# Kernel tuning notes

Hardware: AMD Instinct MI355X
Metric: run time of the kernel (lower is better)

## Reference

```python
import jax, jax.numpy as jnp
import numpy as np

DIM_MODEL = 2048
H, DK, DV, L = 16, 128, 128, 2048
LN_EPS = 1e-5


def setup_inputs() -> dict:
    key = jax.random.key(0)
    ks = jax.random.split(key, 8)
    # xavier-ish scale for weights so softmax logits stay sane
    w_scale = (2.0 / (DIM_MODEL + DK)) ** 0.5
    q = jax.random.normal(ks[0], (1, L, DIM_MODEL), dtype=jnp.float32)
    k = jax.random.normal(ks[1], (1, L, DIM_MODEL), dtype=jnp.float32)
    v = jax.random.normal(ks[2], (1, L, DIM_MODEL), dtype=jnp.float32)
    Wq = jax.random.normal(ks[3], (H, DIM_MODEL, DK), dtype=jnp.float32) * w_scale
    Wk = jax.random.normal(ks[4], (H, DIM_MODEL, DK), dtype=jnp.float32) * w_scale
    Wv = jax.random.normal(ks[5], (H, DIM_MODEL, DV), dtype=jnp.float32) * w_scale
    proj_w = jax.random.normal(ks[6], (H * DV, DIM_MODEL), dtype=jnp.float32) * (1.0 / (H * DV) ** 0.5)
    proj_b = jnp.zeros((DIM_MODEL,), dtype=jnp.float32)
    ln_g = jnp.ones((DIM_MODEL,), dtype=jnp.float32)
    ln_b = jnp.zeros((DIM_MODEL,), dtype=jnp.float32)
    return {"q": q, "k": k, "v": v, "Wq": Wq, "Wk": Wk, "Wv": Wv,
            "proj_w": proj_w, "proj_b": proj_b, "ln_g": ln_g, "ln_b": ln_b}


def reference(q, k, v, Wq, Wk, Wv, proj_w, proj_b, ln_g, ln_b):
    # batch must be 1 (enforced by torch.bmm shape rules in the source)
    residual = q  # (1, L, D)
    qs, kv, vv = q[0], k[0], v[0]  # (L, D)
    dim_model = qs.shape[-1]
    temper = jnp.asarray(dim_model, qs.dtype) ** 0.5  # sqrt(dim_model), NOT sqrt(dk)
    qh = jnp.einsum('ld,hdk->hlk', qs, Wq)  # (H, L, dk)
    kh = jnp.einsum('ld,hdk->hlk', kv, Wk)  # (H, L, dk)
    vh = jnp.einsum('ld,hdv->hlv', vv, Wv)  # (H, L, dv)
    scores = jnp.einsum('hqk,hmk->hqm', qh, kh) / temper  # (H, Lq, Lk)
    # faithful quirk: softmax over dim=1 (the QUERY axis)
    attn = jax.nn.softmax(scores, axis=1)
    # attn_dropout / dropout are identity in eval mode
    out = jnp.einsum('hqm,hmv->hqv', attn, vh)  # (H, Lq, dv)
    # cat(split(out, batch=1, dim=0), dim=-1) == move head axis into features
    Lq = out.shape[1]
    out = jnp.transpose(out, (1, 0, 2)).reshape(Lq, -1)  # (Lq, H*dv)
    out = out @ proj_w + proj_b  # (Lq, dim_model)
    y = out[None] + residual  # (1, Lq, D)
    mu = jnp.mean(y, axis=-1, keepdims=True)
    var = jnp.mean((y - mu) ** 2, axis=-1, keepdims=True)
    y = (y - mu) * jax.lax.rsqrt(var + LN_EPS) * ln_g + ln_b
    return (y, attn)
```

## Files before the change

### kernel.cpp

```cpp
#include <hip/hip_runtime.h>
#include <stdint.h>

#define L 2048
#define DMODEL 2048
#define NH 16

typedef __bf16 bf16x8 __attribute__((ext_vector_type(8)));
typedef float f32x4 __attribute__((ext_vector_type(4)));
typedef short s16x4 __attribute__((ext_vector_type(4)));

__device__ __forceinline__ unsigned short f2bf(float f) {
    union { float f; unsigned int i; } w; w.f = f;
    unsigned int u = w.i;
    unsigned int r = u + 0x7fffu + ((u >> 16) & 1u);
    return (unsigned short)(r >> 16);
}

__device__ __forceinline__ void gload_lds16(const unsigned short* g, unsigned short* l) {
    __builtin_amdgcn_global_load_lds(
        (const __attribute__((address_space(1))) void*)g,
        (__attribute__((address_space(3))) void*)l, 16, 0, 0);
}

template<int CMODE, int AMODE, int BM, int BK, int PSM>
__global__ __launch_bounds__(256, 2)
void gemm_bt(const void* Av,
             const unsigned short* __restrict__ B,
             void* __restrict__ C,
             int M, int N, int K, int lda, int ldb, int ldc,
             long long sA, long long sB, long long sC, float alpha,
             const float* __restrict__ Mg, const float* __restrict__ iLg,
             float* Awr, float* __restrict__ pPart)
{
    static_assert(AMODE != 2 || BM == 64, "softmax-A path assumes BM==64");
    static_assert(PSM == 0 || BM == 128, "PSM partials assume BM==128");
    constexpr int KC8 = BK / 8;
    constexpr int CA  = BM * BK / 2048;
    constexpr int CB  = BK / 16;
    constexpr int MFR = BM / 32;
    constexpr int KG  = BK / 32;

    __shared__ unsigned short As[2][BM * BK];
    __shared__ unsigned short Bs[2][128 * BK];

    const int tid  = threadIdx.x;
    const int wave = tid >> 6;
    const int lane = tid & 63;
    const int quad = lane >> 4;
    const int l16  = lane & 15;

    const int tileN = blockIdx.x * 128;
    const int tileM = blockIdx.y * BM;

    const long long zA = (CMODE == 3) ? (long long)(blockIdx.z >> 4) : (long long)blockIdx.z;
    const unsigned short* A16 = (const unsigned short*)Av + zA * sA;
    const float*          A32 = (const float*)Av + zA * sA;
    B += (long long)blockIdx.z * sB;

    const int wm = (wave >> 1) * (BM / 2);
    const int wn = (wave & 1) * 64;

    float4 fa[CA > 0 ? CA : 1][2];
    float4 m0, m1, l0, l1;
    long long aoff[CA > 0 ? CA : 1];

    auto stageB = [&](int kk, int buf) {
        #pragma unroll
        for (int j = 0; j < CB; ++j) {
            const int ch = tid + j * 256;
            const int rb = ch / KC8, kb = (ch % KC8) * 8;
            gload_lds16(B + (long long)(tileN + rb) * ldb + (kk + kb), &Bs[buf][ch * 8]);
        }
    };
    auto stageA_gl = [&](int kk, int buf) {
        #pragma unroll
        for (int j = 0; j < CA; ++j) {
            const int ch = tid + j * 256;
            const int ra = ch / KC8, ka = (ch % KC8) * 8;
            gload_lds16(A16 + (long long)(tileM + ra) * lda + (kk + ka), &As[buf][ch * 8]);
        }
    };
    auto loadA_sm = [&](int kk) {
        #pragma unroll
        for (int j = 0; j < CA; ++j) {
            const int ch = tid + j * 256;
            const int ra = ch / KC8, ka = (ch % KC8) * 8;
            aoff[j] = (long long)(tileM + ra) * lda + (kk + ka);
            const float* p = A32 + aoff[j];
            fa[j][0] = *(const float4*)p;  fa[j][1] = *(const float4*)(p + 4);
        }
        const int ka = (tid % KC8) * 8;
        const long long sb = (long long)blockIdx.z * 2048 + (kk + ka);
        m0 = *(const float4*)(Mg + sb);  m1 = *(const float4*)(Mg + sb + 4);
        l0 = *(const float4*)(iLg + sb); l1 = *(const float4*)(iLg + sb + 4);
    };
    auto finA_sm = [&](int buf) {
        #pragma unroll
        for (int j = 0; j < CA; ++j) {
            float4 g0 = fa[j][0], g1 = fa[j][1];
            g0.x = __expf(g0.x - m0.x) * l0.x;  g0.y = __expf(g0.y - m0.y) * l0.y;
            g0.z = __expf(g0.z - m0.z) * l0.z;  g0.w = __expf(g0.w - m0.w) * l0.w;
            g1.x = __expf(g1.x - m1.x) * l1.x;  g1.y = __expf(g1.y - m1.y) * l1.y;
            g1.z = __expf(g1.z - m1.z) * l1.z;  g1.w = __expf(g1.w - m1.w) * l1.w;
            float* wb = Awr + (long long)blockIdx.z * sA + aoff[j];
            *(float4*)wb = g0;  *(float4*)(wb + 4) = g1;
            union { int4 v; unsigned short u[8]; } tt;
            tt.u[0] = f2bf(g0.x); tt.u[1] = f2bf(g0.y); tt.u[2] = f2bf(g0.z); tt.u[3] = f2bf(g0.w);
            tt.u[4] = f2bf(g1.x); tt.u[5] = f2bf(g1.y); tt.u[6] = f2bf(g1.z); tt.u[7] = f2bf(g1.w);
            *(int4*)(&As[buf][(tid + j * 256) * 8]) = tt.v;
        }
    };

    f32x4 acc[MFR][4] = {};
    const int nt = K / BK;

    if constexpr (AMODE == 0) {
        stageA_gl(0, 0);
    } else {
        loadA_sm(0);
        finA_sm(0);
    }
    stageB(0, 0);
    __syncthreads();

    int cur = 0;
    for (int t = 0; t < nt; ++t) {
        const int nxt = cur ^ 1;
        const int k0n = (t + 1) * BK;
        const bool pf = (t + 1 < nt);

        if (pf) {
            if constexpr (AMODE == 0) stageA_gl(k0n, nxt);
            else                      loadA_sm(k0n);
            stageB(k0n, nxt);
        }

        bf16x8 af[MFR][KG], bfr[4][KG];
        #pragma unroll
        for (int i = 0; i < MFR; ++i)
            #pragma unroll
            for (int g = 0; g < KG; ++g)
                af[i][g] = *(const bf16x8*)(&As[cur][(wm + i * 16 + l16) * BK + g * 32 + quad * 8]);
        #pragma unroll
        for (int j = 0; j < 4; ++j)
            #pragma unroll
            for (int g = 0; g < KG; ++g)
                bfr[j][g] = *(const bf16x8*)(&Bs[cur][(wn + j * 16 + l16) * BK + g * 32 + quad * 8]);
        #pragma unroll
        for (int g = 0; g < KG; ++g)
            #pragma unroll
            for (int i = 0; i < MFR; ++i)
                #pragma unroll
                for (int j = 0; j < 4; ++j)
                    acc[i][j] = __builtin_amdgcn_mfma_f32_16x16x32_bf16(af[i][g], bfr[j][g], acc[i][j], 0, 0, 0);

        if constexpr (AMODE == 2) { if (pf) finA_sm(nxt); }

        __syncthreads();
        cur = nxt;
    }

    const long long cb = (long long)blockIdx.z * sC;
    const float aEff = (CMODE == 3) ? (blockIdx.z < 16 ? alpha : 1.0f) : alpha;
    #pragma unroll
    for (int i = 0; i < MFR; ++i) {
        const int r0 = tileM + wm + i * 16 + quad * 4;
        #pragma unroll
        for (int j = 0; j < 4; ++j) {
            const int c = tileN + wn + j * 16 + l16;
            f32x4 d = acc[i][j];
            if (CMODE == 0) {
                unsigned short* Cp = (unsigned short*)C + cb;
                #pragma unroll
                for (int r = 0; r < 4; ++r)
                    Cp[(long long)(r0 + r) * ldc + c] = f2bf(d[r] * aEff);
            } else if (CMODE == 1) {
                unsigned short* Cp = (unsigned short*)C + cb + (long long)c * ldc + r0;
                s16x4 pk;
                #pragma unroll
                for (int r = 0; r < 4; ++r) pk[r] = (short)f2bf(d[r] * aEff);
                *(s16x4*)Cp = pk;
            } else if (CMODE == 2) {
                float* Cp = (float*)C + cb;
                #pragma unroll
                for (int r = 0; r < 4; ++r)
                    Cp[(long long)(r0 + r) * ldc + c] = d[r] * aEff;
            } else {
                if (blockIdx.z < 32) {
                    unsigned short* Cp = (unsigned short*)C + cb;
                    #pragma unroll
                    for (int r = 0; r < 4; ++r)
                        Cp[(long long)(r0 + r) * 128 + c] = f2bf(d[r] * aEff);
                } else {
                    unsigned short* Cp = (unsigned short*)C + cb + (long long)c * 2048 + r0;
                    s16x4 pk;
                    #pragma unroll
                    for (int r = 0; r < 4; ++r) pk[r] = (short)f2bf(d[r]);
                    *(s16x4*)Cp = pk;
                }
            }
        }
    }

    if constexpr (PSM) {
        __shared__ float shPm[2][128], shPe[2][128];
        const int wmh = wave >> 1;
        #pragma unroll
        for (int j = 0; j < 4; ++j) {
            float mj = -1e30f;
            #pragma unroll
            for (int i = 0; i < MFR; ++i)
                #pragma unroll
                for (int r = 0; r < 4; ++r) mj = fmaxf(mj, acc[i][j][r]);
            float ej = 0.f;
            #pragma unroll
            for (int i = 0; i < MFR; ++i)
                #pragma unroll
                for (int r = 0; r < 4; ++r) ej += __expf(acc[i][j][r] - mj);
            #pragma unroll
            for (int off = 16; off < 64; off <<= 1) {
                float mo = __shfl_xor(mj, off, 64);
                float eo = __shfl_xor(ej, off, 64);
                float mn = fmaxf(mj, mo);
                ej = ej * __expf(mj - mn) + eo * __expf(mo - mn);
                mj = mn;
            }
            if (quad == 0) {
                shPm[wmh][wn + j * 16 + l16] = mj;
                shPe[wmh][wn + j * 16 + l16] = ej;
            }
        }
        __syncthreads();
        if (tid < 128) {
            const float mA = shPm[0][tid], mB = shPm[1][tid];
            const float m = fmaxf(mA, mB);
            const float e = shPe[0][tid] * __expf(mA - m) + shPe[1][tid] * __expf(mB - m);
            const long long pidx = ((long long)blockIdx.z * 16 + blockIdx.y) * 2048 + tileN + tid;
            pPart[pidx] = m;
            pPart[pidx + 16 * 16 * 2048] = e;
        }
    }
}

__global__ __launch_bounds__(256)
void colstats(const float* __restrict__ pPart, float* __restrict__ Mg,
              float* __restrict__ iLg)
{
    const int c = blockIdx.x * 256 + threadIdx.x;
    const int h = blockIdx.y;
    const float* pm = pPart + (long long)h * 16 * 2048 + c;
    const float* pe = pm + 16 * 16 * 2048;
    float M = -1e30f;
    #pragma unroll
    for (int b = 0; b < 16; ++b) M = fmaxf(M, pm[b * 2048]);
    float Ls = 0.f;
    #pragma unroll
    for (int b = 0; b < 16; ++b) Ls += pe[b * 2048] * __expf(pm[b * 2048] - M);
    Mg[h * 2048 + c]  = M;
    iLg[h * 2048 + c] = 1.0f / Ls;
}

__global__ __launch_bounds__(256)
void cvt_f2b3(const float* __restrict__ a, const float* __restrict__ b,
              const float* __restrict__ c, unsigned short* __restrict__ out)
{
    const float* in = blockIdx.z == 0 ? a : blockIdx.z == 1 ? b : c;
    const long long i = ((long long)blockIdx.x * 256 + threadIdx.x) * 8;
    const float4 f0 = *(const float4*)(in + i);
    const float4 f1 = *(const float4*)(in + i + 4);
    union { int4 v; unsigned short u[8]; } t;
    t.u[0] = f2bf(f0.x); t.u[1] = f2bf(f0.y); t.u[2] = f2bf(f0.z); t.u[3] = f2bf(f0.w);
    t.u[4] = f2bf(f1.x); t.u[5] = f2bf(f1.y); t.u[6] = f2bf(f1.z); t.u[7] = f2bf(f1.w);
    *(int4*)(out + (long long)blockIdx.z * 4194304 + i) = t.v;
}

__global__ __launch_bounds__(256)
void transpose_f2b(const float* __restrict__ in, unsigned short* __restrict__ out,
                   int rows, int cols)
{
    __shared__ float t[32][33];
    const long long base = (long long)blockIdx.z * rows * cols;
    const int c0 = blockIdx.x * 32, r0 = blockIdx.y * 32;
    const int tx = threadIdx.x, ty0 = threadIdx.y;
    #pragma unroll
    for (int jj = 0; jj < 4; ++jj) {
        const int j = ty0 + jj * 8;
        t[j][tx] = in[base + (long long)(r0 + j) * cols + (c0 + tx)];
    }
    __syncthreads();
    #pragma unroll
    for (int jj = 0; jj < 4; ++jj) {
        const int j = ty0 + jj * 8;
        out[base + (long long)(c0 + j) * rows + (r0 + tx)] = f2bf(t[tx][j]);
    }
}

__global__ __launch_bounds__(256)
void transpose_f2b3(const float* __restrict__ Wq, const float* __restrict__ Wk,
                    const float* __restrict__ Wv, unsigned short* __restrict__ out)
{
    __shared__ float t[32][33];
    const int z = blockIdx.z, widx = z >> 4, h = z & 15;
    const float* in = (widx == 0 ? Wq : widx == 1 ? Wk : Wv) + (long long)h * 2048 * 128;
    unsigned short* o = out + (long long)z * 262144;
    const int c0 = blockIdx.x * 32, r0 = blockIdx.y * 32;
    const int tx = threadIdx.x, ty0 = threadIdx.y;
    #pragma unroll
    for (int jj = 0; jj < 4; ++jj) {
        const int j = ty0 + jj * 8;
        t[j][tx] = in[(long long)(r0 + j) * 128 + (c0 + tx)];
    }
    __syncthreads();
    #pragma unroll
    for (int jj = 0; jj < 4; ++jj) {
        const int j = ty0 + jj * 8;
        o[(long long)(c0 + j) * 2048 + (r0 + tx)] = f2bf(t[tx][j]);
    }
}

__global__ __launch_bounds__(256)
void ln_resid(const float* __restrict__ ypre, const float* __restrict__ resid,
              const float* __restrict__ pb, const float* __restrict__ g,
              const float* __restrict__ bta, float* __restrict__ y)
{
    __shared__ float as_[4], as2_[4];
    const int l = blockIdx.x;
    const int tid = threadIdx.x;
    float v[8]; float s = 0.f, s2 = 0.f;
    #pragma unroll
    for (int i = 0; i < 8; ++i) {
        const int d = tid + i * 256;
        float t = ypre[(long long)l * DMODEL + d] + pb[d] + resid[(long long)l * DMODEL + d];
        v[i] = t; s += t; s2 += t * t;
    }
    #pragma unroll
    for (int off = 32; off > 0; off >>= 1) {
        s  += __shfl_down(s, off, 64);
        s2 += __shfl_down(s2, off, 64);
    }
    const int wave = tid >> 6, lane = tid & 63;
    if (lane == 0) { as_[wave] = s; as2_[wave] = s2; }
    __syncthreads();
    const float S  = as_[0] + as_[1] + as_[2] + as_[3];
    const float S2 = as2_[0] + as2_[1] + as2_[2] + as2_[3];
    const float mu  = S * (1.0f / DMODEL);
    const float var = S2 * (1.0f / DMODEL) - mu * mu;
    const float rs  = rsqrtf(var + 1e-5f);
    #pragma unroll
    for (int i = 0; i < 8; ++i) {
        const int d = tid + i * 256;
        y[(long long)l * DMODEL + d] = (v[i] - mu) * rs * g[d] + bta[d];
    }
}

extern "C" void kernel_launch(void* const* d_in, const int* in_sizes, int n_in,
                              void* d_out, int out_size, void* d_ws, size_t ws_size,
                              hipStream_t stream)
{
    const float* q  = (const float*)d_in[0];
    const float* k  = (const float*)d_in[1];
    const float* v  = (const float*)d_in[2];
    const float* Wq = (const float*)d_in[3];
    const float* Wk = (const float*)d_in[4];
    const float* Wv = (const float*)d_in[5];
    const float* Pw = (const float*)d_in[6];
    const float* Pb = (const float*)d_in[7];
    const float* Lg = (const float*)d_in[8];
    const float* Lb = (const float*)d_in[9];

    float* y    = (float*)d_out;
    float* attn = y + (size_t)L * DMODEL;

    const size_t SEG = (size_t)4194304;
    unsigned short* T0  = (unsigned short*)d_ws;
    unsigned short* qh  = T0 + SEG;
    unsigned short* kh  = qh + SEG;
    unsigned short* vhT = kh + SEG;
    unsigned short* O   = vhT + SEG;
    float* ypre  = (float*)qh;
    float* pPart = (float*)d_ws;
    float* Mg    = pPart + 2 * 16 * 16 * 2048;
    float* iLg   = Mg + 16 * 2048;

    unsigned short* qkvb = (unsigned short*)attn;
    unsigned short* WT   = qkvb + 3 * SEG;

    const float inv_temper = 0.022097086912079608f;
    dim3 tb(32, 8);

    cvt_f2b3<<<dim3(2048, 1, 3), 256, 0, stream>>>(q, k, v, qkvb);
    transpose_f2b3<<<dim3(4, 64, 48), tb, 0, stream>>>(Wq, Wk, Wv, WT);

    gemm_bt<3, 0, 128, 32, 0><<<dim3(1, 16, 48), 256, 0, stream>>>(qkvb, WT, qh,
        2048, 128, 2048, 2048, 2048, 0, 4194304LL, 262144LL, 262144LL, inv_temper,
        nullptr, nullptr, nullptr, nullptr);

    gemm_bt<2, 0, 128, 32, 1><<<dim3(16, 16, 16), 256, 0, stream>>>(qh, kh, attn,
        2048, 2048, 128, 128, 128, 2048, 262144LL, 262144LL, 4194304LL, 1.0f,
        nullptr, nullptr, nullptr, pPart);

    colstats<<<dim3(8, NH), 256, 0, stream>>>(pPart, Mg, iLg);

    gemm_bt<0, 2, 64, 64, 0><<<dim3(1, 32, 16), 256, 0, stream>>>(attn, vhT, O,
        2048, 128, 2048, 2048, 2048, 2048, 4194304LL, 262144LL, 128LL, 1.0f,
        Mg, iLg, attn, nullptr);

    transpose_f2b<<<dim3(64, 64, 1), tb, 0, stream>>>(Pw, T0, 2048, 2048);
    gemm_bt<2, 0, 64, 64, 0><<<dim3(16, 32, 1), 256, 0, stream>>>(O, T0, (void*)ypre,
        2048, 2048, 2048, 2048, 2048, 2048, 0LL, 0LL, 0LL, 1.0f,
        nullptr, nullptr, nullptr, nullptr);

    ln_resid<<<dim3(2048), 256, 0, stream>>>(ypre, q, Pb, Lg, Lb, y);
}
```

Measured before the change: 639.4 us.

## Fuse score recomputation, softmax normalization and PV into one kernel

```diff
diff --git a/kernel.cpp b/kernel.cpp
--- a/kernel.cpp
+++ b/kernel.cpp
@@ -22,18 +22,15 @@
         (__attribute__((address_space(3))) void*)l, 16, 0, 0);
 }
 
-template<int CMODE, int AMODE, int BM, int BK, int PSM>
+template<int CMODE, int BM, int BK, int PSM>
 __global__ __launch_bounds__(256, 2)
-void gemm_bt(const void* Av,
+void gemm_bt(const unsigned short* __restrict__ Ag,
              const unsigned short* __restrict__ B,
              void* __restrict__ C,
-             int M, int N, int K, int lda, int ldb, int ldc,
+             int K, int lda, int ldb, int ldc,
              long long sA, long long sB, long long sC, float alpha,
-             const float* __restrict__ Mg, const float* __restrict__ iLg,
-             float* Awr, float* __restrict__ pPart)
-{
-    static_assert(AMODE != 2 || BM == 64, "softmax-A path assumes BM==64");
-    static_assert(PSM == 0 || BM == 128, "PSM partials assume BM==128");
+             float* __restrict__ pPart)
+{
     constexpr int KC8 = BK / 8;
     constexpr int CA  = BM * BK / 2048;
     constexpr int CB  = BK / 16;
@@ -53,16 +50,11 @@
     const int tileM = blockIdx.y * BM;
 
     const long long zA = (CMODE == 3) ? (long long)(blockIdx.z >> 4) : (long long)blockIdx.z;
-    const unsigned short* A16 = (const unsigned short*)Av + zA * sA;
-    const float*          A32 = (const float*)Av + zA * sA;
+    const unsigned short* A16 = Ag + zA * sA;
     B += (long long)blockIdx.z * sB;
 
     const int wm = (wave >> 1) * (BM / 2);
     const int wn = (wave & 1) * 64;
-
-    float4 fa[CA > 0 ? CA : 1][2];
-    float4 m0, m1, l0, l1;
-    long long aoff[CA > 0 ? CA : 1];
 
     auto stageB = [&](int kk, int buf) {
         #pragma unroll
@@ -72,7 +64,7 @@
             gload_lds16(B + (long long)(tileN + rb) * ldb + (kk + kb), &Bs[buf][ch * 8]);
         }
     };
-    auto stageA_gl = [&](int kk, int buf) {
+    auto stageA = [&](int kk, int buf) {
         #pragma unroll
         for (int j = 0; j < CA; ++j) {
             const int ch = tid + j * 256;
@@ -80,46 +72,11 @@
             gload_lds16(A16 + (long long)(tileM + ra) * lda + (kk + ka), &As[buf][ch * 8]);
         }
     };
-    auto loadA_sm = [&](int kk) {
-        #pragma unroll
-        for (int j = 0; j < CA; ++j) {
-            const int ch = tid + j * 256;
-            const int ra = ch / KC8, ka = (ch % KC8) * 8;
-            aoff[j] = (long long)(tileM + ra) * lda + (kk + ka);
-            const float* p = A32 + aoff[j];
-            fa[j][0] = *(const float4*)p;  fa[j][1] = *(const float4*)(p + 4);
-        }
-        const int ka = (tid % KC8) * 8;
-        const long long sb = (long long)blockIdx.z * 2048 + (kk + ka);
-        m0 = *(const float4*)(Mg + sb);  m1 = *(const float4*)(Mg + sb + 4);
-        l0 = *(const float4*)(iLg + sb); l1 = *(const float4*)(iLg + sb + 4);
-    };
-    auto finA_sm = [&](int buf) {
-        #pragma unroll
-        for (int j = 0; j < CA; ++j) {
-            float4 g0 = fa[j][0], g1 = fa[j][1];
-            g0.x = __expf(g0.x - m0.x) * l0.x;  g0.y = __expf(g0.y - m0.y) * l0.y;
-            g0.z = __expf(g0.z - m0.z) * l0.z;  g0.w = __expf(g0.w - m0.w) * l0.w;
-            g1.x = __expf(g1.x - m1.x) * l1.x;  g1.y = __expf(g1.y - m1.y) * l1.y;
-            g1.z = __expf(g1.z - m1.z) * l1.z;  g1.w = __expf(g1.w - m1.w) * l1.w;
-            float* wb = Awr + (long long)blockIdx.z * sA + aoff[j];
-            *(float4*)wb = g0;  *(float4*)(wb + 4) = g1;
-            union { int4 v; unsigned short u[8]; } tt;
-            tt.u[0] = f2bf(g0.x); tt.u[1] = f2bf(g0.y); tt.u[2] = f2bf(g0.z); tt.u[3] = f2bf(g0.w);
-            tt.u[4] = f2bf(g1.x); tt.u[5] = f2bf(g1.y); tt.u[6] = f2bf(g1.z); tt.u[7] = f2bf(g1.w);
-            *(int4*)(&As[buf][(tid + j * 256) * 8]) = tt.v;
-        }
-    };
 
     f32x4 acc[MFR][4] = {};
     const int nt = K / BK;
 
-    if constexpr (AMODE == 0) {
-        stageA_gl(0, 0);
-    } else {
-        loadA_sm(0);
-        finA_sm(0);
-    }
+    stageA(0, 0);
     stageB(0, 0);
     __syncthreads();
 
@@ -127,13 +84,7 @@
     for (int t = 0; t < nt; ++t) {
         const int nxt = cur ^ 1;
         const int k0n = (t + 1) * BK;
-        const bool pf = (t + 1 < nt);
-
-        if (pf) {
-            if constexpr (AMODE == 0) stageA_gl(k0n, nxt);
-            else                      loadA_sm(k0n);
-            stageB(k0n, nxt);
-        }
+        if (t + 1 < nt) { stageA(k0n, nxt); stageB(k0n, nxt); }
 
         bf16x8 af[MFR][KG], bfr[4][KG];
         #pragma unroll
@@ -154,49 +105,49 @@
                 for (int j = 0; j < 4; ++j)
                     acc[i][j] = __builtin_amdgcn_mfma_f32_16x16x32_bf16(af[i][g], bfr[j][g], acc[i][j], 0, 0, 0);
 
-        if constexpr (AMODE == 2) { if (pf) finA_sm(nxt); }
-
         __syncthreads();
         cur = nxt;
     }
 
     const long long cb = (long long)blockIdx.z * sC;
     const float aEff = (CMODE == 3) ? (blockIdx.z < 16 ? alpha : 1.0f) : alpha;
-    #pragma unroll
-    for (int i = 0; i < MFR; ++i) {
-        const int r0 = tileM + wm + i * 16 + quad * 4;
-        #pragma unroll
-        for (int j = 0; j < 4; ++j) {
-            const int c = tileN + wn + j * 16 + l16;
-            f32x4 d = acc[i][j];
-            if (CMODE == 0) {
-                unsigned short* Cp = (unsigned short*)C + cb;
-                #pragma unroll
-                for (int r = 0; r < 4; ++r)
-                    Cp[(long long)(r0 + r) * ldc + c] = f2bf(d[r] * aEff);
-            } else if (CMODE == 1) {
-                unsigned short* Cp = (unsigned short*)C + cb + (long long)c * ldc + r0;
-                s16x4 pk;
-                #pragma unroll
-                for (int r = 0; r < 4; ++r) pk[r] = (short)f2bf(d[r] * aEff);
-                *(s16x4*)Cp = pk;
-            } else if (CMODE == 2) {
-                float* Cp = (float*)C + cb;
-                #pragma unroll
-                for (int r = 0; r < 4; ++r)
-                    Cp[(long long)(r0 + r) * ldc + c] = d[r] * aEff;
-            } else {
-                if (blockIdx.z < 32) {
+    if constexpr (CMODE != 4) {
+        #pragma unroll
+        for (int i = 0; i < MFR; ++i) {
+            const int r0 = tileM + wm + i * 16 + quad * 4;
+            #pragma unroll
+            for (int j = 0; j < 4; ++j) {
+                const int c = tileN + wn + j * 16 + l16;
+                f32x4 d = acc[i][j];
+                if (CMODE == 0) {
                     unsigned short* Cp = (unsigned short*)C + cb;
                     #pragma unroll
                     for (int r = 0; r < 4; ++r)
-                        Cp[(long long)(r0 + r) * 128 + c] = f2bf(d[r] * aEff);
-                } else {
-                    unsigned short* Cp = (unsigned short*)C + cb + (long long)c * 2048 + r0;
+                        Cp[(long long)(r0 + r) * ldc + c] = f2bf(d[r] * aEff);
+                } else if (CMODE == 1) {
+                    unsigned short* Cp = (unsigned short*)C + cb + (long long)c * ldc + r0;
                     s16x4 pk;
                     #pragma unroll
-                    for (int r = 0; r < 4; ++r) pk[r] = (short)f2bf(d[r]);
+                    for (int r = 0; r < 4; ++r) pk[r] = (short)f2bf(d[r] * aEff);
                     *(s16x4*)Cp = pk;
+                } else if (CMODE == 2) {
+                    float* Cp = (float*)C + cb;
+                    #pragma unroll
+                    for (int r = 0; r < 4; ++r)
+                        Cp[(long long)(r0 + r) * ldc + c] = d[r] * aEff;
+                } else {
+                    if (blockIdx.z < 32) {
+                        unsigned short* Cp = (unsigned short*)C + cb;
+                        #pragma unroll
+                        for (int r = 0; r < 4; ++r)
+                            Cp[(long long)(r0 + r) * 128 + c] = f2bf(d[r] * aEff);
+                    } else {
+                        unsigned short* Cp = (unsigned short*)C + cb + (long long)c * 2048 + r0;
+                        s16x4 pk;
+                        #pragma unroll
+                        for (int r = 0; r < 4; ++r) pk[r] = (short)f2bf(d[r]);
+                        *(s16x4*)Cp = pk;
+                    }
                 }
             }
         }
@@ -242,6 +193,148 @@
     }
 }
 
+__global__ __launch_bounds__(256, 2)
+void fused_pv(const unsigned short* __restrict__ qh,
+              const unsigned short* __restrict__ kh,
+              const unsigned short* __restrict__ vhT,
+              const float* __restrict__ Mg, const float* __restrict__ iLg,
+              float* __restrict__ attn, unsigned short* __restrict__ O)
+{
+    __shared__ unsigned short qh_s[128 * 128];
+    __shared__ unsigned short kh_s[2][32 * 128];
+    __shared__ unsigned short vh_s[2][128 * 32];
+    __shared__ unsigned short p16[2][128 * 32];
+
+    const int tid = threadIdx.x;
+    const int wave = tid >> 6, lane = tid & 63, quad = lane >> 4, l16 = lane & 15;
+    const int qt = blockIdx.x, h = blockIdx.y;
+    const int wA = wave >> 1, wB = wave & 1;
+    const unsigned short* qg = qh + (long long)h * 262144 + (long long)qt * 128 * 128;
+    const unsigned short* kg = kh + (long long)h * 262144;
+    const unsigned short* vg = vhT + (long long)h * 262144;
+    const float* mgp = Mg + h * 2048;
+    const float* ilp = iLg + h * 2048;
+    float* ap = attn + (long long)h * L * L + (long long)qt * 128 * 2048;
+
+    auto stage_kv = [&](int kt, int buf) {
+        #pragma unroll
+        for (int jj = 0; jj < 2; ++jj) {
+            const int c = tid + jj * 256;
+            const int rl = c >> 4, sl = (c & 15) ^ (rl & 7);
+            gload_lds16(kg + (long long)(kt * 32 + rl) * 128 + sl * 8, &kh_s[buf][c * 8]);
+        }
+        #pragma unroll
+        for (int jj = 0; jj < 2; ++jj) {
+            const int c = tid + jj * 256;
+            const int vd = c >> 2, sl = (c & 3) ^ (vd & 3);
+            gload_lds16(vg + (long long)vd * 2048 + kt * 32 + sl * 8, &vh_s[buf][c * 8]);
+        }
+    };
+
+    #pragma unroll
+    for (int jj = 0; jj < 8; ++jj) {
+        const int c = tid + jj * 256;
+        const int rl = c >> 4, sl = (c & 15) ^ (rl & 7);
+        gload_lds16(qg + (long long)rl * 128 + sl * 8, &qh_s[c * 8]);
+    }
+    stage_kv(0, 0);
+    __syncthreads();
+
+    f32x4 acc_o[4][4] = {};
+    const int krow = wA * 16 + l16;
+
+    for (int t = 0; t < 64; ++t) {
+        const int cb = t & 1;
+        if (t > 0) {
+            const int pb = cb ^ 1;
+            bf16x8 pa[4], vb[4];
+            #pragma unroll
+            for (int i = 0; i < 4; ++i) {
+                const int q = wA * 64 + i * 16 + l16;
+                pa[i] = *(const bf16x8*)(&p16[pb][q * 32 + ((quad * 8) ^ ((q & 3) << 3))]);
+            }
+            #pragma unroll
+            for (int j = 0; j < 4; ++j) {
+                const int vd = wB * 64 + j * 16 + l16;
+                vb[j] = *(const bf16x8*)(&vh_s[pb][vd * 32 + ((quad * 8) ^ ((vd & 3) << 3))]);
+            }
+            #pragma unroll
+            for (int i = 0; i < 4; ++i)
+                #pragma unroll
+                for (int j = 0; j < 4; ++j)
+                    acc_o[i][j] = __builtin_amdgcn_mfma_f32_16x16x32_bf16(pa[i], vb[j], acc_o[i][j], 0, 0, 0);
+        }
+        __builtin_amdgcn_sched_barrier(0);
+        if (t < 63) stage_kv(t + 1, cb ^ 1);
+
+        bf16x8 af[4];
+        #pragma unroll
+        for (int g = 0; g < 4; ++g)
+            af[g] = *(const bf16x8*)(&kh_s[cb][krow * 128 + ((g * 32 + quad * 8) ^ ((krow & 7) << 3))]);
+        f32x4 acc_s[4];
+        #pragma unroll
+        for (int j = 0; j < 4; ++j) {
+            const int q = wB * 64 + j * 16 + l16;
+            f32x4 s = {};
+            #pragma unroll
+            for (int g = 0; g < 4; ++g) {
+                bf16x8 bq = *(const bf16x8*)(&qh_s[q * 128 + ((g * 32 + quad * 8) ^ ((q & 7) << 3))]);
+                s = __builtin_amdgcn_mfma_f32_16x16x32_bf16(af[g], bq, s, 0, 0, 0);
+            }
+            acc_s[j] = s;
+        }
+
+        const int kb = t * 32 + wA * 16 + quad * 4;
+        const f32x4 mg4 = *(const f32x4*)(mgp + kb);
+        const f32x4 il4 = *(const f32x4*)(ilp + kb);
+        #pragma unroll
+        for (int j = 0; j < 4; ++j) {
+            const int q = wB * 64 + j * 16 + l16;
+            f32x4 p;
+            #pragma unroll
+            for (int r = 0; r < 4; ++r)
+                p[r] = __expf(acc_s[j][r] - mg4[r]) * il4[r];
+            *(f32x4*)(ap + (long long)q * 2048 + kb) = p;
+            s16x4 pk;
+            #pragma unroll
+            for (int r = 0; r < 4; ++r) pk[r] = (short)f2bf(p[r]);
+            *(s16x4*)(&p16[cb][q * 32 + ((wA * 16 + quad * 4) ^ ((q & 3) << 3))]) = pk;
+        }
+        __syncthreads();
+    }
+
+    {
+        bf16x8 pa[4], vb[4];
+        #pragma unroll
+        for (int i = 0; i < 4; ++i) {
+            const int q = wA * 64 + i * 16 + l16;
+            pa[i] = *(const bf16x8*)(&p16[1][q * 32 + ((quad * 8) ^ ((q & 3) << 3))]);
+        }
+        #pragma unroll
+        for (int j = 0; j < 4; ++j) {
+            const int vd = wB * 64 + j * 16 + l16;
+            vb[j] = *(const bf16x8*)(&vh_s[1][vd * 32 + ((quad * 8) ^ ((vd & 3) << 3))]);
+        }
+        #pragma unroll
+        for (int i = 0; i < 4; ++i)
+            #pragma unroll
+            for (int j = 0; j < 4; ++j)
+                acc_o[i][j] = __builtin_amdgcn_mfma_f32_16x16x32_bf16(pa[i], vb[j], acc_o[i][j], 0, 0, 0);
+    }
+
+    #pragma unroll
+    for (int i = 0; i < 4; ++i) {
+        const int q = qt * 128 + wA * 64 + i * 16 + quad * 4;
+        #pragma unroll
+        for (int j = 0; j < 4; ++j) {
+            const int vd = h * 128 + wB * 64 + j * 16 + l16;
+            #pragma unroll
+            for (int r = 0; r < 4; ++r)
+                O[(long long)(q + r) * 2048 + vd] = f2bf(acc_o[i][j][r]);
+        }
+    }
+}
+
 __global__ __launch_bounds__(256)
 void colstats(const float* __restrict__ pPart, float* __restrict__ Mg,
               float* __restrict__ iLg)
@@ -391,24 +484,19 @@
     cvt_f2b3<<<dim3(2048, 1, 3), 256, 0, stream>>>(q, k, v, qkvb);
     transpose_f2b3<<<dim3(4, 64, 48), tb, 0, stream>>>(Wq, Wk, Wv, WT);
 
-    gemm_bt<3, 0, 128, 32, 0><<<dim3(1, 16, 48), 256, 0, stream>>>(qkvb, WT, qh,
-        2048, 128, 2048, 2048, 2048, 0, 4194304LL, 262144LL, 262144LL, inv_temper,
-        nullptr, nullptr, nullptr, nullptr);
-
-    gemm_bt<2, 0, 128, 32, 1><<<dim3(16, 16, 16), 256, 0, stream>>>(qh, kh, attn,
-        2048, 2048, 128, 128, 128, 2048, 262144LL, 262144LL, 4194304LL, 1.0f,
-        nullptr, nullptr, nullptr, pPart);
+    gemm_bt<3, 128, 32, 0><<<dim3(1, 16, 48), 256, 0, stream>>>(qkvb, WT, qh,
+        2048, 2048, 2048, 0, 4194304LL, 262144LL, 262144LL, inv_temper, nullptr);
+
+    gemm_bt<4, 128, 32, 1><<<dim3(16, 16, 16), 256, 0, stream>>>(qh, kh, nullptr,
+        128, 128, 128, 0, 262144LL, 262144LL, 0LL, 1.0f, pPart);
 
     colstats<<<dim3(8, NH), 256, 0, stream>>>(pPart, Mg, iLg);
 
-    gemm_bt<0, 2, 64, 64, 0><<<dim3(1, 32, 16), 256, 0, stream>>>(attn, vhT, O,
-        2048, 128, 2048, 2048, 2048, 2048, 4194304LL, 262144LL, 128LL, 1.0f,
-        Mg, iLg, attn, nullptr);
+    fused_pv<<<dim3(16, NH), 256, 0, stream>>>(qh, kh, vhT, Mg, iLg, attn, O);
 
     transpose_f2b<<<dim3(64, 64, 1), tb, 0, stream>>>(Pw, T0, 2048, 2048);
-    gemm_bt<2, 0, 64, 64, 0><<<dim3(16, 32, 1), 256, 0, stream>>>(O, T0, (void*)ypre,
-        2048, 2048, 2048, 2048, 2048, 2048, 0LL, 0LL, 0LL, 1.0f,
-        nullptr, nullptr, nullptr, nullptr);
+    gemm_bt<2, 64, 64, 0><<<dim3(16, 32, 1), 256, 0, stream>>>(O, T0, (void*)ypre,
+        2048, 2048, 2048, 2048, 0LL, 0LL, 0LL, 1.0f, nullptr);
 
     ln_resid<<<dim3(2048), 256, 0, stream>>>(ypre, q, Pb, Lg, Lb, y);
 }
```

Result: faster. 596.7 us (-6.7%).
